# Optimization experiments

Measured on AMD Instinct MI355X. Metric: run time of the kernel, lower is better.

Reference implementation:

```python
import jax, jax.numpy as jnp
import numpy as np

B, IN, OUT, D = 8192, 1024, 1024, 8


def setup_inputs() -> dict:
    key = jax.random.key(0)
    k1, k2, k3, k4 = jax.random.split(key, 4)
    # kaiming-uniform-ish init for weights, uniform for biases (values don't affect correctness)
    bound = 1.0 / np.sqrt(IN)
    return {
        "input": jax.random.normal(k1, (B, IN), dtype=jnp.float32),
        "w": jax.random.uniform(k2, (B, D), dtype=jnp.float32),
        "weights": jax.random.uniform(k3, (D, OUT, IN), dtype=jnp.float32, minval=-bound, maxval=bound),
        "biases": jax.random.uniform(k4, (D, OUT), dtype=jnp.float32, minval=-bound, maxval=bound),
    }


def reference(input, w, weights, biases):
    # Original math: weight[b] = sum_d w[b,d] * weights[d]  (shape [out,in])
    #                out[b]    = input[b] @ weight[b].T + sum_d w[b,d]*biases[d]
    # Restructured as one big GEMM + cheap dsize reduction:
    # tmp[b,d,o] = sum_i input[b,i] * weights[d,o,i]   (GEMM: [B,in] x [in, d*out])
    tmp = jnp.einsum('bi,doi->bdo', input, weights)
    out = jnp.einsum('bdo,bd->bo', tmp, w) + w @ biases
    return out
```

## Files before the change

kernel.cpp:

```cpp
#include <hip/hip_runtime.h>
#include <stdint.h>

typedef unsigned short u16;
typedef float v4f __attribute__((ext_vector_type(4)));
typedef short v8s __attribute__((ext_vector_type(8)));

#define B_   8192
#define IN_  1024
#define OUT_ 1024
#define D_   8

#define BM 128
#define BN 128
#define BK 64

__device__ __forceinline__ u16 f2bf(float f) {
  uint32_t u = __float_as_uint(f);
  u += 0x7fffu + ((u >> 16) & 1u);
  return (u16)(u >> 16);
}

__device__ __forceinline__ uint32_t cvtpk(float lo, float hi) {
  uint32_t r;
  asm("v_cvt_pk_bf16_f32 %0, %1, %2" : "=v"(r) : "v"(lo), "v"(hi));
  return r;
}

__global__ __launch_bounds__(256) void convert_w(
    const float* __restrict__ weights, u16* __restrict__ wtBf) {
  const int i4 = blockIdx.x * 256 + threadIdx.x;
  float4 v = ((const float4*)weights)[i4];
  ushort4 o;
  o.x = f2bf(v.x); o.y = f2bf(v.y); o.z = f2bf(v.z); o.w = f2bf(v.w);
  ((ushort4*)wtBf)[i4] = o;
}

__device__ __forceinline__ void gload_lds16(const u16* g, u16* l) {
  typedef __attribute__((address_space(1))) void gvoid;
  typedef __attribute__((address_space(3))) void lvoid;
  __builtin_amdgcn_global_load_lds((gvoid*)g, (lvoid*)l, 16, 0, 0);
}

__global__ __launch_bounds__(256, 2) void gemm_fused(
    const float* __restrict__ Ain,
    const u16* __restrict__ Wt,
    const float* __restrict__ w,
    const float* __restrict__ biases,
    float* __restrict__ out) {
  __shared__ __align__(16) u16 As[2][BM * BK];
  __shared__ __align__(16) u16 Bs[3][BN * BK];

  const int id   = blockIdx.x;
  const int bx   = id & 7;
  const int by   = id >> 3;

  const int tid  = threadIdx.x;
  const int wid  = tid >> 6;
  const int lane = tid & 63;
  const int wr   = wid >> 1, wc = wid & 1;
  const int quad = lane >> 4, l16 = lane & 15;
  const int m0   = by * BM;
  const int n0   = bx * BN;

  const int swz  = (lane & 7) ^ ((lane >> 3) & 7);
  const int rowS = wid * 32 + (lane >> 3);
  const float* aBase[4];
  const u16*   bBase[4];
  int cOff[4];
#pragma unroll
  for (int j = 0; j < 4; ++j) {
    const int row = rowS + j * 8;
    aBase[j] = Ain + (size_t)(m0 + row) * IN_ + swz * 8;
    bBase[j] = Wt  + (size_t)(n0 + row) * IN_ + swz * 8;
    cOff[j]  = (wid * 256 + j * 64 + lane) * 8;
  }

  float4 wA[4], wB[4];
#pragma unroll
  for (int j = 0; j < 4; ++j) {
    const float* wp = w + (size_t)(m0 + rowS + j * 8) * D_;
    wA[j] = ((const float4*)wp)[0];
    wB[j] = ((const float4*)wp)[1];
  }

  const int aRow = wr * 64 + l16;
  const int bRow = wc * 64 + l16;
  const int e    = l16 & 7;
  int aC[2];
#pragma unroll
  for (int h = 0; h < 2; ++h) aC[h] = ((quad + 4 * h) ^ e) * 8;

  const v4f vzero = {0.f, 0.f, 0.f, 0.f};
  v4f acc[4][4];
#pragma unroll
  for (int mt = 0; mt < 4; ++mt)
#pragma unroll
    for (int nt = 0; nt < 4; ++nt) acc[mt][nt] = vzero;

  u16* bC = Bs[0];
  u16* bN = Bs[1];
  u16* bS = Bs[2];

  float4 a0[4], a1[4];

#pragma unroll
  for (int j = 0; j < 4; ++j) {
    const float4* ap = (const float4*)aBase[j];
    a0[j] = ap[0]; a1[j] = ap[1];
  }
#pragma unroll
  for (int j = 0; j < 4; ++j) gload_lds16(bBase[j], bC + cOff[j]);
#pragma unroll
  for (int j = 0; j < 4; ++j)
    gload_lds16(bBase[j] + (size_t)(OUT_ * IN_), bN + cOff[j]);
#pragma unroll
  for (int j = 0; j < 4; ++j) {
    const float s = wA[j].x;
    uint4 pk;
    pk.x = cvtpk(a0[j].x * s, a0[j].y * s);
    pk.y = cvtpk(a0[j].z * s, a0[j].w * s);
    pk.z = cvtpk(a1[j].x * s, a1[j].y * s);
    pk.w = cvtpk(a1[j].z * s, a1[j].w * s);
    *(uint4*)(&As[0][cOff[j]]) = pk;
  }
  asm volatile("s_waitcnt vmcnt(4) lgkmcnt(0)" ::: "memory");
  __builtin_amdgcn_s_barrier();

  for (int it = 0; it < IN_ / BK; ++it) {
#pragma unroll
    for (int dd = 0; dd < D_; ++dd) {
      const int cur = dd & 1;
      const int nxt = cur ^ 1;
      const bool lastPhase = (it == 15) && (dd == 7);

      if (dd == 6) {
#pragma unroll
        for (int j = 0; j < 4; ++j) {
          const float s = wB[j].w;
          uint4 pk;
          pk.x = cvtpk(a0[j].x * s, a0[j].y * s);
          pk.y = cvtpk(a0[j].z * s, a0[j].w * s);
          pk.z = cvtpk(a1[j].x * s, a1[j].y * s);
          pk.w = cvtpk(a1[j].z * s, a1[j].w * s);
          *(uint4*)(&As[nxt][cOff[j]]) = pk;
        }
        if (it < 15) {
#pragma unroll
          for (int j = 0; j < 4; ++j) {
            const float4* ap = (const float4*)(aBase[j] + (it + 1) * BK);
            a0[j] = ap[0]; a1[j] = ap[1];
          }
        }
      }

      if (!((it == 15) && (dd >= 6))) {
        const int sdd2 = (dd <= 5) ? dd + 2 : dd - 6;
        const int sit2 = (dd <= 5) ? it : it + 1;
#pragma unroll
        for (int j = 0; j < 4; ++j)
          gload_lds16(bBase[j] + (size_t)sdd2 * (OUT_ * IN_) + sit2 * BK,
                      bS + cOff[j]);
      }

      __builtin_amdgcn_s_setprio(1);
#pragma unroll
      for (int h = 0; h < 2; ++h) {
        v8s af[4], bf[4];
#pragma unroll
        for (int mt = 0; mt < 4; ++mt)
          af[mt] = *(const v8s*)(&As[cur][(aRow + mt * 16) * BK + aC[h]]);
#pragma unroll
        for (int nt = 0; nt < 4; ++nt)
          bf[nt] = *(const v8s*)(bC + (bRow + nt * 16) * BK + aC[h]);
#pragma unroll
        for (int mt = 0; mt < 4; ++mt)
#pragma unroll
          for (int nt = 0; nt < 4; ++nt)
            acc[mt][nt] = __builtin_amdgcn_mfma_f32_16x16x32_bf16(
                af[mt], bf[nt], acc[mt][nt], 0, 0, 0);
      }
      __builtin_amdgcn_s_setprio(0);

      if (dd != 6 && !lastPhase) {
        const int sdd = (dd + 1) & 7;
#pragma unroll
        for (int j = 0; j < 4; ++j) {
          const float s = (sdd < 4) ? wA[j][sdd] : wB[j][sdd - 4];
          uint4 pk;
          pk.x = cvtpk(a0[j].x * s, a0[j].y * s);
          pk.y = cvtpk(a0[j].z * s, a0[j].w * s);
          pk.z = cvtpk(a1[j].x * s, a1[j].y * s);
          pk.w = cvtpk(a1[j].z * s, a1[j].w * s);
          *(uint4*)(&As[nxt][cOff[j]]) = pk;
        }
      }

      if (!lastPhase) {
        if (dd == 6) {
          if (it < 15)
            asm volatile("s_waitcnt vmcnt(12) lgkmcnt(0)" ::: "memory");
          else
            asm volatile("s_waitcnt vmcnt(0) lgkmcnt(0)" ::: "memory");
        } else {
          asm volatile("s_waitcnt vmcnt(4) lgkmcnt(0)" ::: "memory");
        }
        __builtin_amdgcn_s_barrier();
      }

      u16* tmp = bC; bC = bN; bN = bS; bS = tmp;
    }
  }

  float bcol[4][8];
#pragma unroll
  for (int nt = 0; nt < 4; ++nt) {
    const int col = n0 + wc * 64 + nt * 16 + l16;
#pragma unroll
    for (int dd = 0; dd < 8; ++dd) bcol[nt][dd] = biases[dd * OUT_ + col];
  }
#pragma unroll
  for (int mt = 0; mt < 4; ++mt) {
#pragma unroll
    for (int r = 0; r < 4; ++r) {
      const int grow = m0 + wr * 64 + mt * 16 + quad * 4 + r;
      const v4f* wp = (const v4f*)(w + (size_t)grow * D_);
      const v4f wa = wp[0], wb = wp[1];
#pragma unroll
      for (int nt = 0; nt < 4; ++nt) {
        const int col = n0 + wc * 64 + nt * 16 + l16;
        const float bias = wa[0] * bcol[nt][0] + wa[1] * bcol[nt][1] +
                           wa[2] * bcol[nt][2] + wa[3] * bcol[nt][3] +
                           wb[0] * bcol[nt][4] + wb[1] * bcol[nt][5] +
                           wb[2] * bcol[nt][6] + wb[3] * bcol[nt][7];
        out[(size_t)grow * OUT_ + col] = acc[mt][nt][r] + bias;
      }
    }
  }
}

extern "C" void kernel_launch(void* const* d_in, const int* in_sizes, int n_in,
                              void* d_out, int out_size, void* d_ws, size_t ws_size,
                              hipStream_t stream) {
  const float* input   = (const float*)d_in[0];
  const float* w       = (const float*)d_in[1];
  const float* weights = (const float*)d_in[2];
  const float* biases  = (const float*)d_in[3];
  float* out = (float*)d_out;

  u16* wtBf = (u16*)d_ws;

  const int nF4 = (D_ * OUT_ * IN_) / 4;
  convert_w<<<dim3(nF4 / 256), 256, 0, stream>>>(weights, wtBf);
  gemm_fused<<<dim3(512), 256, 0, stream>>>(input, wtBf, w, biases, out);
}
```

Baseline: 233.8 us.

## Enlarge block tile to 256x128 with 8 waves and two-half interleaved schedule

Doubles the M tile to 256 rows and uses 512 threads (8 waves), launching 256 blocks instead of 512. The B buffer becomes a 4-deep ring and each D-step is split into two halves. Each half interleaves LDS reads, A-staging, one B prefetch and 16 MFMAs, with barriers in between, so memory traffic is spread across the compute. This aims to halve the B traffic per output and overlap staging with MFMA better. The cost is about 128KB of LDS per block, which limits each CU to one block, plus extra barriers per step.

After: 279.5 us. 1.2x slower.

```diff
diff --git a/kernel.cpp b/kernel.cpp
--- a/kernel.cpp
+++ b/kernel.cpp
@@ -10,7 +10,7 @@
 #define OUT_ 1024
 #define D_   8
 
-#define BM 128
+#define BM 256
 #define BN 128
 #define BK 64
 
@@ -41,14 +41,14 @@
   __builtin_amdgcn_global_load_lds((gvoid*)g, (lvoid*)l, 16, 0, 0);
 }
 
-__global__ __launch_bounds__(256, 2) void gemm_fused(
+__global__ __launch_bounds__(512, 2) void gemm_8p(
     const float* __restrict__ Ain,
     const u16* __restrict__ Wt,
     const float* __restrict__ w,
     const float* __restrict__ biases,
     float* __restrict__ out) {
   __shared__ __align__(16) u16 As[2][BM * BK];
-  __shared__ __align__(16) u16 Bs[3][BN * BK];
+  __shared__ __align__(16) u16 Bs[4][BN * BK];
 
   const int id   = blockIdx.x;
   const int bx   = id & 7;
@@ -62,23 +62,27 @@
   const int m0   = by * BM;
   const int n0   = bx * BN;
 
-  const int swz  = (lane & 7) ^ ((lane >> 3) & 7);
-  const int rowS = wid * 32 + (lane >> 3);
+  const int swz   = (lane & 7) ^ ((lane >> 3) & 7);
+  const int rowSA = wid * 32 + (lane >> 3);
+  const int rowSB = wid * 16 + (lane >> 3);
   const float* aBase[4];
-  const u16*   bBase[4];
-  int cOff[4];
+  const u16*   bBase[2];
+  int aOffL[4], bOffL[2];
 #pragma unroll
   for (int j = 0; j < 4; ++j) {
-    const int row = rowS + j * 8;
-    aBase[j] = Ain + (size_t)(m0 + row) * IN_ + swz * 8;
-    bBase[j] = Wt  + (size_t)(n0 + row) * IN_ + swz * 8;
-    cOff[j]  = (wid * 256 + j * 64 + lane) * 8;
+    aBase[j] = Ain + (size_t)(m0 + rowSA + j * 8) * IN_ + swz * 8;
+    aOffL[j] = (wid * 256 + j * 64 + lane) * 8;
+  }
+#pragma unroll
+  for (int j = 0; j < 2; ++j) {
+    bBase[j] = Wt + (size_t)(n0 + rowSB + j * 8) * IN_ + swz * 8;
+    bOffL[j] = (wid * 128 + j * 64 + lane) * 8;
   }
 
   float4 wA[4], wB[4];
 #pragma unroll
   for (int j = 0; j < 4; ++j) {
-    const float* wp = w + (size_t)(m0 + rowS + j * 8) * D_;
+    const float* wp = w + (size_t)(m0 + rowSA + j * 8) * D_;
     wA[j] = ((const float4*)wp)[0];
     wB[j] = ((const float4*)wp)[1];
   }
@@ -97,11 +101,36 @@
 #pragma unroll
     for (int nt = 0; nt < 4; ++nt) acc[mt][nt] = vzero;
 
-  u16* bC = Bs[0];
-  u16* bN = Bs[1];
-  u16* bS = Bs[2];
-
   float4 a0[4], a1[4];
+
+#define STAGE_A(bufA, jj, s_)                                   \
+  {                                                             \
+    const float s = (s_);                                       \
+    uint4 pk;                                                   \
+    pk.x = cvtpk(a0[jj].x * s, a0[jj].y * s);                   \
+    pk.y = cvtpk(a0[jj].z * s, a0[jj].w * s);                   \
+    pk.z = cvtpk(a1[jj].x * s, a1[jj].y * s);                   \
+    pk.w = cvtpk(a1[jj].z * s, a1[jj].w * s);                   \
+    *(uint4*)(&As[bufA][aOffL[jj]]) = pk;                       \
+  }
+#define WSEL(jj, sdd) ((sdd) < 4 ? wA[jj][(sdd)] : wB[jj][(sdd)-4])
+
+#define DS_READ(bufA, bufB, h)                                          \
+  _Pragma("unroll") for (int mt = 0; mt < 4; ++mt)                      \
+    af[mt] = *(const v8s*)(&As[bufA][(aRow + mt * 16) * BK + aC[h]]);   \
+  _Pragma("unroll") for (int nt = 0; nt < 4; ++nt)                      \
+    bf[nt] = *(const v8s*)(&Bs[bufB][(bRow + nt * 16) * BK + aC[h]]);
+
+#define MFMA16()                                                        \
+  __builtin_amdgcn_s_barrier();                                         \
+  asm volatile("s_waitcnt lgkmcnt(0)" ::: "memory");                    \
+  __builtin_amdgcn_sched_barrier(0);                                    \
+  __builtin_amdgcn_s_setprio(1);                                        \
+  _Pragma("unroll") for (int mt = 0; mt < 4; ++mt)                      \
+    _Pragma("unroll") for (int nt = 0; nt < 4; ++nt)                    \
+      acc[mt][nt] = __builtin_amdgcn_mfma_f32_16x16x32_bf16(            \
+          af[mt], bf[nt], acc[mt][nt], 0, 0, 0);                        \
+  __builtin_amdgcn_s_setprio(0);
 
 #pragma unroll
   for (int j = 0; j < 4; ++j) {
@@ -109,105 +138,74 @@
     a0[j] = ap[0]; a1[j] = ap[1];
   }
 #pragma unroll
-  for (int j = 0; j < 4; ++j) gload_lds16(bBase[j], bC + cOff[j]);
-#pragma unroll
-  for (int j = 0; j < 4; ++j)
-    gload_lds16(bBase[j] + (size_t)(OUT_ * IN_), bN + cOff[j]);
-#pragma unroll
-  for (int j = 0; j < 4; ++j) {
-    const float s = wA[j].x;
-    uint4 pk;
-    pk.x = cvtpk(a0[j].x * s, a0[j].y * s);
-    pk.y = cvtpk(a0[j].z * s, a0[j].w * s);
-    pk.z = cvtpk(a1[j].x * s, a1[j].y * s);
-    pk.w = cvtpk(a1[j].z * s, a1[j].w * s);
-    *(uint4*)(&As[0][cOff[j]]) = pk;
-  }
-  asm volatile("s_waitcnt vmcnt(4) lgkmcnt(0)" ::: "memory");
+  for (int j = 0; j < 2; ++j) gload_lds16(bBase[j], &Bs[0][bOffL[j]]);
+#pragma unroll
+  for (int j = 0; j < 2; ++j)
+    gload_lds16(bBase[j] + (size_t)(OUT_ * IN_), &Bs[1][bOffL[j]]);
+#pragma unroll
+  for (int j = 0; j < 4; ++j) STAGE_A(0, j, wA[j].x);
+  asm volatile("s_waitcnt vmcnt(2) lgkmcnt(0)" ::: "memory");
   __builtin_amdgcn_s_barrier();
 
   for (int it = 0; it < IN_ / BK; ++it) {
 #pragma unroll
     for (int dd = 0; dd < D_; ++dd) {
-      const int cur = dd & 1;
-      const int nxt = cur ^ 1;
-      const bool lastPhase = (it == 15) && (dd == 7);
-
-      if (dd == 6) {
-#pragma unroll
-        for (int j = 0; j < 4; ++j) {
-          const float s = wB[j].w;
-          uint4 pk;
-          pk.x = cvtpk(a0[j].x * s, a0[j].y * s);
-          pk.y = cvtpk(a0[j].z * s, a0[j].w * s);
-          pk.z = cvtpk(a1[j].x * s, a1[j].y * s);
-          pk.w = cvtpk(a1[j].z * s, a1[j].w * s);
-          *(uint4*)(&As[nxt][cOff[j]]) = pk;
+      const int cA = dd & 1, nA = cA ^ 1;
+      const int cB = dd & 3, sB = (dd + 2) & 3;
+      const int sdd1 = (dd + 1) & 7;
+      const int sdd2 = (dd + 2) & 7;
+      const bool lastTile  = (it == 15) && (dd == 7);
+      const bool skipBload = (it == 15) && (dd >= 6);
+      const int  sit2 = (dd >= 6) ? it + 1 : it;
+
+      {
+        v8s af[4], bf[4];
+        DS_READ(cA, cB, 0);
+        if (dd == 6) {
+#pragma unroll
+          for (int j = 0; j < 4; ++j) STAGE_A(nA, j, WSEL(j, 7));
+        } else if (!lastTile) {
+#pragma unroll
+          for (int j = 0; j < 2; ++j) STAGE_A(nA, j, WSEL(j, sdd1));
         }
-        if (it < 15) {
-#pragma unroll
-          for (int j = 0; j < 4; ++j) {
-            const float4* ap = (const float4*)(aBase[j] + (it + 1) * BK);
-            a0[j] = ap[0]; a1[j] = ap[1];
+        if (!skipBload)
+          gload_lds16(bBase[0] + (size_t)sdd2 * (OUT_ * IN_) + sit2 * BK,
+                      &Bs[sB][bOffL[0]]);
+        MFMA16();
+        __builtin_amdgcn_s_barrier();
+      }
+
+      {
+        v8s af[4], bf[4];
+        DS_READ(cA, cB, 1);
+        if (dd == 6) {
+          if (it < 15) {
+#pragma unroll
+            for (int j = 0; j < 4; ++j) {
+              const float4* ap = (const float4*)(aBase[j] + (it + 1) * BK);
+              a0[j] = ap[0]; a1[j] = ap[1];
+            }
           }
+        } else if (!lastTile) {
+#pragma unroll
+          for (int j = 2; j < 4; ++j) STAGE_A(nA, j, WSEL(j, sdd1));
+        }
+        if (!skipBload)
+          gload_lds16(bBase[1] + (size_t)sdd2 * (OUT_ * IN_) + sit2 * BK,
+                      &Bs[sB][bOffL[1]]);
+        MFMA16();
+        if (!lastTile) {
+          if (dd == 6) {
+            if (it < 15)
+              asm volatile("s_waitcnt vmcnt(10)" ::: "memory");
+            else
+              asm volatile("s_waitcnt vmcnt(0)" ::: "memory");
+          } else {
+            asm volatile("s_waitcnt vmcnt(2)" ::: "memory");
+          }
+          __builtin_amdgcn_s_barrier();
         }
       }
-
-      if (!((it == 15) && (dd >= 6))) {
-        const int sdd2 = (dd <= 5) ? dd + 2 : dd - 6;
-        const int sit2 = (dd <= 5) ? it : it + 1;
-#pragma unroll
-        for (int j = 0; j < 4; ++j)
-          gload_lds16(bBase[j] + (size_t)sdd2 * (OUT_ * IN_) + sit2 * BK,
-                      bS + cOff[j]);
-      }
-
-      __builtin_amdgcn_s_setprio(1);
-#pragma unroll
-      for (int h = 0; h < 2; ++h) {
-        v8s af[4], bf[4];
-#pragma unroll
-        for (int mt = 0; mt < 4; ++mt)
-          af[mt] = *(const v8s*)(&As[cur][(aRow + mt * 16) * BK + aC[h]]);
-#pragma unroll
-        for (int nt = 0; nt < 4; ++nt)
-          bf[nt] = *(const v8s*)(bC + (bRow + nt * 16) * BK + aC[h]);
-#pragma unroll
-        for (int mt = 0; mt < 4; ++mt)
-#pragma unroll
-          for (int nt = 0; nt < 4; ++nt)
-            acc[mt][nt] = __builtin_amdgcn_mfma_f32_16x16x32_bf16(
-                af[mt], bf[nt], acc[mt][nt], 0, 0, 0);
-      }
-      __builtin_amdgcn_s_setprio(0);
-
-      if (dd != 6 && !lastPhase) {
-        const int sdd = (dd + 1) & 7;
-#pragma unroll
-        for (int j = 0; j < 4; ++j) {
-          const float s = (sdd < 4) ? wA[j][sdd] : wB[j][sdd - 4];
-          uint4 pk;
-          pk.x = cvtpk(a0[j].x * s, a0[j].y * s);
-          pk.y = cvtpk(a0[j].z * s, a0[j].w * s);
-          pk.z = cvtpk(a1[j].x * s, a1[j].y * s);
-          pk.w = cvtpk(a1[j].z * s, a1[j].w * s);
-          *(uint4*)(&As[nxt][cOff[j]]) = pk;
-        }
-      }
-
-      if (!lastPhase) {
-        if (dd == 6) {
-          if (it < 15)
-            asm volatile("s_waitcnt vmcnt(12) lgkmcnt(0)" ::: "memory");
-          else
-            asm volatile("s_waitcnt vmcnt(0) lgkmcnt(0)" ::: "memory");
-        } else {
-          asm volatile("s_waitcnt vmcnt(4) lgkmcnt(0)" ::: "memory");
-        }
-        __builtin_amdgcn_s_barrier();
-      }
-
-      u16* tmp = bC; bC = bN; bN = bS; bS = tmp;
     }
   }
 
@@ -251,5 +249,5 @@
 
   const int nF4 = (D_ * OUT_ * IN_) / 4;
   convert_w<<<dim3(nF4 / 256), 256, 0, stream>>>(weights, wtBf);
-  gemm_fused<<<dim3(512), 256, 0, stream>>>(input, wtBf, w, biases, out);
-}
+  gemm_8p<<<dim3(256), 512, 0, stream>>>(input, wtBf, w, biases, out);
+}
```
